# Kernel tuning notes

Hardware: AMD Instinct MI355X
Metric: run time of the kernel (lower is better)

## Reference

```python
import jax, jax.numpy as jnp
import numpy as np

B, Q, KV = 8, 16, 2048
NQ, NK, NV, H = 512, 512, 512, 512

def setup_inputs() -> dict:
    key = jax.random.key(0)
    k = jax.random.split(key, 7)
    s = 0.02
    return {
        "query": jax.random.normal(k[0], (B, Q, NQ), jnp.float32),
        "keys": jax.random.normal(k[1], (B, KV, NK), jnp.float32),
        "values": jax.random.normal(k[2], (B, KV, NV), jnp.float32),
        "W_weight": jax.random.normal(k[3], (H, NQ + NK), jnp.float32) * s,
        "W_bias": jax.random.normal(k[4], (H,), jnp.float32) * s,
        "v_weight": jax.random.normal(k[5], (1, H), jnp.float32) * s,
        "v_bias": jax.random.normal(k[6], (1,), jnp.float32) * s,
    }

def reference(query, keys, values, W_weight, W_bias, v_weight, v_bias):
    # Split W over the concat axis: cat([query, keys]) @ W^T == query@Wq^T + keys@Wk^T
    Wq = W_weight[:, :NQ]   # [H, Nq]
    Wk = W_weight[:, NQ:]   # [H, Nk]
    q_part = jnp.einsum('bqn,hn->bqh', query, Wq)   # [B,Q,H]
    k_part = jnp.einsum('bkn,hn->bkh', keys, Wk)    # [B,KV,H]
    # broadcast-add -> [B,KV,Q,H], tanh, project to scalar energy
    energy = jnp.tanh(k_part[:, :, None, :] + q_part[:, None, :, :] + W_bias)
    e = jnp.einsum('bkqh,h->bkq', energy, v_weight[0]) + v_bias[0]  # [B,KV,Q]
    scores = jax.nn.softmax(e, axis=1)              # softmax over KV
    # output = (values^T @ scores)^T -> [B,Q,Nv]
    output = jnp.einsum('bkn,bkq->bqn', values, scores)
    return output
```

## Files before the change

### kernel.cpp

```cpp
#include <hip/hip_runtime.h>
#include <cstddef>

using bf16x8  = __attribute__((ext_vector_type(8))) short;
using f32x4   = __attribute__((ext_vector_type(4))) float;
using ushort8 = __attribute__((ext_vector_type(8))) unsigned short;

#define GLL16(gp, lp) __builtin_amdgcn_global_load_lds( \
    (const __attribute__((address_space(1))) unsigned int*)(const void*)(gp), \
    (__attribute__((address_space(3))) unsigned int*)(void*)(lp), 16, 0, 0)

__device__ __forceinline__ float exp2_f(float x){ float r; asm("v_exp_f32 %0, %1" : "=v"(r) : "v"(x)); return r; }
__device__ __forceinline__ float rcp_f (float x){ float r; asm("v_rcp_f32 %0, %1" : "=v"(r) : "v"(x)); return r; }
__device__ __forceinline__ unsigned pk2(float lo, float hi){
  unsigned r; asm("v_cvt_pk_bf16_f32 %0, %1, %2" : "=v"(r) : "v"(lo), "v"(hi)); return r;
}
__device__ __forceinline__ unsigned short f2bf(float f){
  unsigned int u = __float_as_uint(f);
  u = u + 0x7FFFu + ((u >> 16) & 1u);
  return (unsigned short)(u >> 16);
}

#define KEYS_N   8388608
#define QG_BLOCKS 16
#define CONV_BLOCKS 4224
#define SCALE_2LOG2E 2.885390081777927f

#define OFF_KEYS_BF   0u
#define OFF_WK_BF     16777216u
#define OFF_EQB       17301504u
#define OFF_EPART     17563648u
#define OFF_SC        21757952u

__global__ __launch_bounds__(256) void k_convert(
    const float* __restrict__ keys, const float* __restrict__ W,
    const float* __restrict__ query,
    unsigned short* __restrict__ keys_bf, unsigned short* __restrict__ wk_bf,
    float* __restrict__ eqb)
{
  __shared__ short qg[128*32 + 32*32];
  if (blockIdx.x < QG_BLOCKS) {
    const int n0 = blockIdx.x * 32;
    const int tid = threadIdx.x;
    const int l = tid & 63, w = tid >> 6;
    short* A  = qg;
    short* Bs = qg + 4096;
    const int sub = tid >> 3;
    const int c4  = (tid & 7) * 4;
    const int wm = w & 1, wn = w >> 1;
    const int fr = l & 15, fg = l >> 4;

    f32x4 acc[4];
    #pragma unroll
    for (int i = 0; i < 4; ++i) acc[i] = (f32x4){0.f,0.f,0.f,0.f};

    float4 a4[4], b4, a4n[4], b4n;
    #pragma unroll
    for (int m = 0; m < 4; ++m)
      a4[m] = *(const float4*)(query + (size_t)(m * 32 + sub) * 512 + c4);
    b4 = *(const float4*)(W + (size_t)(n0 + sub) * 1024 + c4);

    for (int kt = 0; kt < 16; ++kt) {
      if (kt < 15) {
        const int k0 = (kt + 1) * 32;
        #pragma unroll
        for (int m = 0; m < 4; ++m)
          a4n[m] = *(const float4*)(query + (size_t)(m * 32 + sub) * 512 + k0 + c4);
        b4n = *(const float4*)(W + (size_t)(n0 + sub) * 1024 + k0 + c4);
      }
      __syncthreads();
      #pragma unroll
      for (int m = 0; m < 4; ++m) {
        const int row = m * 32 + sub;
        const int o = row * 32 + (((c4 >> 3) ^ ((row >> 1) & 3)) << 3) + (c4 & 7);
        *(uint2*)&A[o] = make_uint2(pk2(a4[m].x, a4[m].y), pk2(a4[m].z, a4[m].w));
      }
      {
        const int o = sub * 32 + (((c4 >> 3) ^ ((sub >> 1) & 3)) << 3) + (c4 & 7);
        *(uint2*)&Bs[o] = make_uint2(pk2(b4.x, b4.y), pk2(b4.z, b4.w));
      }
      __syncthreads();
      bf16x8 af[4], bfv;
      #pragma unroll
      for (int i = 0; i < 4; ++i) {
        const int ar = wm*64 + i*16 + fr;
        af[i] = *(const bf16x8*)&A[ar*32 + ((fg ^ ((ar>>1)&3)) << 3)];
      }
      const int br = wn*16 + fr;
      bfv = *(const bf16x8*)&Bs[br*32 + ((fg ^ ((br>>1)&3)) << 3)];
      #pragma unroll
      for (int i = 0; i < 4; ++i)
        acc[i] = __builtin_amdgcn_mfma_f32_16x16x32_bf16(af[i], bfv, acc[i], 0, 0, 0);
      if (kt < 15) {
        #pragma unroll
        for (int m = 0; m < 4; ++m) a4[m] = a4n[m];
        b4 = b4n;
      }
    }
    const int gh = n0 + wn*16 + fr;
    #pragma unroll
    for (int i = 0; i < 4; ++i)
      #pragma unroll
      for (int r = 0; r < 4; ++r) {
        const int gm = wm*64 + i*16 + fg*4 + r;
        eqb[gm * 512 + gh] = exp2_f(acc[i][r] * SCALE_2LOG2E);
      }
    return;
  }
  int idx = ((blockIdx.x - QG_BLOCKS) * 256 + threadIdx.x) * 8;
  const float* src;
  unsigned short* dst;
  if (idx < KEYS_N) { src = keys + idx; dst = keys_bf + idx; }
  else {
    int e = idx - KEYS_N;
    src = W + (size_t)(e >> 9) * 1024 + 512 + (e & 511);
    dst = wk_bf + e;
  }
  float4 a = *(const float4*)src;
  float4 b = *(const float4*)(src + 4);
  ushort8 o;
  o[0]=f2bf(a.x); o[1]=f2bf(a.y); o[2]=f2bf(a.z); o[3]=f2bf(a.w);
  o[4]=f2bf(b.x); o[5]=f2bf(b.y); o[6]=f2bf(b.z); o[7]=f2bf(b.w);
  *(ushort8*)dst = o;
}

struct FusedSM {
  union {
    struct { short A[2][8192]; short B[2][8192]; } g;
    float ekf[128 * 128];
  } u;
};

__global__ __launch_bounds__(256, 2) void k_fused(
    const unsigned short* __restrict__ keys_bf, const unsigned short* __restrict__ wk_bf,
    const float* __restrict__ w_bias, const float* __restrict__ eqb,
    const float* __restrict__ vw, float* __restrict__ e_part)
{
  __shared__ FusedSM sm;
  const int tid = threadIdx.x;
  const int l = tid & 63, w = tid >> 6;
  const int by = blockIdx.x;
  const int hc = blockIdx.y;
  const int h0 = hc * 128;
  const int b  = by >> 4;

  const unsigned short* Aptr = keys_bf + (size_t)by * 128 * 512;
  const unsigned short* Bptr = wk_bf + (size_t)h0 * 512;

  const int srow = w * 32 + (l >> 3);
  const int scol = ((l & 7) ^ (l >> 3)) * 8;
  const int wm = w >> 1, wn = w & 1;
  const int fr = l & 15, fg = l >> 4;
  const int axk = fr & 7;

  f32x4 acc[4][4];
  #pragma unroll
  for (int i = 0; i < 4; ++i)
    #pragma unroll
    for (int j = 0; j < 4; ++j) acc[i][j] = (f32x4){0.f,0.f,0.f,0.f};

  auto stage = [&](int buf, int kt) {
    const int k0 = kt * 64;
    #pragma unroll
    for (int r = 0; r < 4; ++r) {
      GLL16(Aptr + (srow + r * 8) * 512 + k0 + scol, &sm.u.g.A[buf][w * 2048 + r * 512]);
      GLL16(Bptr + (srow + r * 8) * 512 + k0 + scol, &sm.u.g.B[buf][w * 2048 + r * 512]);
    }
  };
  auto compute = [&](int buf) {
    #pragma unroll
    for (int ks = 0; ks < 2; ++ks) {
      bf16x8 af[4], bfv[4];
      #pragma unroll
      for (int i = 0; i < 4; ++i) {
        af[i]  = *(const bf16x8*)&sm.u.g.A[buf][(wm*64 + i*16 + fr) * 64 + ((ks*4 + fg) ^ axk) * 8];
        bfv[i] = *(const bf16x8*)&sm.u.g.B[buf][(wn*64 + i*16 + fr) * 64 + ((ks*4 + fg) ^ axk) * 8];
      }
      #pragma unroll
      for (int i = 0; i < 4; ++i)
        #pragma unroll
        for (int j = 0; j < 4; ++j)
          acc[i][j] = __builtin_amdgcn_mfma_f32_16x16x32_bf16(af[i], bfv[j], acc[i][j], 0, 0, 0);
    }
  };

  stage(0, 0);
  #pragma unroll 1
  for (int kt = 0; kt < 8; ++kt) {
    if (kt < 7) {
      stage((kt + 1) & 1, kt + 1);
      asm volatile("s_waitcnt vmcnt(8)" ::: "memory");
    } else {
      asm volatile("s_waitcnt vmcnt(0)" ::: "memory");
    }
    __builtin_amdgcn_sched_barrier(0);
    __builtin_amdgcn_s_barrier();
    __builtin_amdgcn_sched_barrier(0);
    compute(kt & 1);
    asm volatile("s_waitcnt lgkmcnt(0)" ::: "memory");
    __builtin_amdgcn_sched_barrier(0);
    __builtin_amdgcn_s_barrier();
    __builtin_amdgcn_sched_barrier(0);
  }

  #pragma unroll
  for (int j = 0; j < 4; ++j) {
    const int col = wn*64 + j*16 + fr;
    const float bias = w_bias[h0 + col];
    const int chunk = col >> 3, coff = col & 7;
    #pragma unroll
    for (int i = 0; i < 4; ++i)
      #pragma unroll
      for (int r = 0; r < 4; ++r) {
        const int row = wm*64 + i*16 + fg*4 + r;
        const int key = ((row & 3) << 2) | ((row >> 2) & 3);
        sm.u.ekf[row * 128 + ((chunk ^ key) << 3) + coff] =
            exp2_f((acc[i][j][r] + bias) * SCALE_2LOG2E);
      }
  }

  const int ql = l >> 2, g = l & 3;
  float eq[32], vv[32];
  #pragma unroll
  for (int s = 0; s < 4; ++s)
    #pragma unroll
    for (int hf = 0; hf < 2; ++hf) {
      const int c = h0 + s*32 + hf*16 + g*4;
      const float4 e4 = *(const float4*)(eqb + (size_t)(b * 16 + ql) * 512 + c);
      const float4 v4 = *(const float4*)(vw + c);
      const int o = s*8 + hf*4;
      eq[o+0]=e4.x; eq[o+1]=e4.y; eq[o+2]=e4.z; eq[o+3]=e4.w;
      vv[o+0]=-2.f*v4.x; vv[o+1]=-2.f*v4.y; vv[o+2]=-2.f*v4.z; vv[o+3]=-2.f*v4.w;
    }
  __syncthreads();

  #pragma unroll 2
  for (int kk = 0; kk < 16; ++kk) {
    const int k0 = w * 32 + kk, k1 = k0 + 16;
    const int key = ((kk & 3) << 2) | ((kk >> 2) & 3);
    float a0 = 0.f, a1 = 0.f;
    #pragma unroll
    for (int s = 0; s < 4; ++s)
      #pragma unroll
      for (int hf = 0; hf < 2; ++hf) {
        const int ck = (4*s + 2*hf + (g >> 1)) ^ key;
        const int off = (ck << 3) + (g & 1) * 4;
        const float4 E0 = *(const float4*)&sm.u.ekf[k0 * 128 + off];
        const float4 E1 = *(const float4*)&sm.u.ekf[k1 * 128 + off];
        const int o = s*8 + hf*4;
        a0 = fmaf(vv[o+0], rcp_f(fmaf(E0.x, eq[o+0], 1.f)), a0);
        a0 = fmaf(vv[o+1], rcp_f(fmaf(E0.y, eq[o+1], 1.f)), a0);
        a0 = fmaf(vv[o+2], rcp_f(fmaf(E0.z, eq[o+2], 1.f)), a0);
        a0 = fmaf(vv[o+3], rcp_f(fmaf(E0.w, eq[o+3], 1.f)), a0);
        a1 = fmaf(vv[o+0], rcp_f(fmaf(E1.x, eq[o+0], 1.f)), a1);
        a1 = fmaf(vv[o+1], rcp_f(fmaf(E1.y, eq[o+1], 1.f)), a1);
        a1 = fmaf(vv[o+2], rcp_f(fmaf(E1.z, eq[o+2], 1.f)), a1);
        a1 = fmaf(vv[o+3], rcp_f(fmaf(E1.w, eq[o+3], 1.f)), a1);
      }
    a0 += __shfl_xor(a0, 1, 64);
    a0 += __shfl_xor(a0, 2, 64);
    a1 += __shfl_xor(a1, 1, 64);
    a1 += __shfl_xor(a1, 2, 64);
    if (g == 0) {
      e_part[(size_t)hc * 262144 + ((size_t)(by * 128 + k0)) * 16 + ql] = a0;
      e_part[(size_t)hc * 262144 + ((size_t)(by * 128 + k1)) * 16 + ql] = a1;
    }
  }
}

__global__ __launch_bounds__(256) void k_softmax(
    const float* __restrict__ e_part, float* __restrict__ sc)
{
  const int b = blockIdx.x >> 4, q = blockIdx.x & 15;
  const int base = b * 32768 + q;
  const int tid = threadIdx.x;
  __shared__ float redm[4], reds[4];

  float vals[8];
  float mx = -1e30f;
  #pragma unroll
  for (int i = 0; i < 8; ++i) {
    const int x = base + (tid + i * 256) * 16;
    vals[i] = (e_part[x] + e_part[x + 262144]) + (e_part[x + 524288] + e_part[x + 786432]);
    mx = fmaxf(mx, vals[i]);
  }
  #pragma unroll
  for (int msk = 1; msk < 64; msk <<= 1) mx = fmaxf(mx, __shfl_xor(mx, msk, 64));
  if ((tid & 63) == 0) redm[tid >> 6] = mx;
  __syncthreads();
  mx = fmaxf(fmaxf(redm[0], redm[1]), fmaxf(redm[2], redm[3]));

  float ex[8], sum = 0.f;
  #pragma unroll
  for (int i = 0; i < 8; ++i) { ex[i] = __expf(vals[i] - mx); sum += ex[i]; }
  #pragma unroll
  for (int msk = 1; msk < 64; msk <<= 1) sum += __shfl_xor(sum, msk, 64);
  if ((tid & 63) == 0) reds[tid >> 6] = sum;
  __syncthreads();
  sum = reds[0] + reds[1] + reds[2] + reds[3];
  const float r = 1.f / sum;
  #pragma unroll
  for (int i = 0; i < 8; ++i) sc[base + (tid + i * 256) * 16] = ex[i] * r;
}

__global__ __launch_bounds__(512) void k_pv(
    const float* __restrict__ values, const float* __restrict__ sc,
    float* __restrict__ out)
{
  __shared__ float lds[128 * 20];
  const int tid = threadIdx.x;
  const int nc = blockIdx.x & 31, b = blockIdx.x >> 5;
  const int n = tid & 15, kg = tid >> 4;
  const int l = tid & 63, w = tid >> 6;
  const int n0 = nc * 16;

  float acc[16];
  #pragma unroll
  for (int q = 0; q < 16; ++q) acc[q] = 0.f;

  for (int kc = 0; kc < 16; ++kc) {
    __syncthreads();
    {
      const float* ssrc = sc + (size_t)(b * 2048 + kc * 128) * 16;
      const int row = tid >> 2, c4 = (tid & 3) * 4;
      *(float4*)&lds[row * 20 + c4] = *(const float4*)&ssrc[row * 16 + c4];
    }
    __syncthreads();
    const float* vb = values + ((size_t)(b * 2048 + kc * 128 + kg * 4)) * 512 + n0 + n;
    #pragma unroll
    for (int k2 = 0; k2 < 4; ++k2) {
      const float v = vb[(size_t)k2 * 512];
      const float* sr = &lds[(kg * 4 + k2) * 20];
      #pragma unroll
      for (int qq = 0; qq < 4; ++qq) {
        const float4 s4 = *(const float4*)&sr[qq * 4];
        acc[qq*4+0] = fmaf(v, s4.x, acc[qq*4+0]);
        acc[qq*4+1] = fmaf(v, s4.y, acc[qq*4+1]);
        acc[qq*4+2] = fmaf(v, s4.z, acc[qq*4+2]);
        acc[qq*4+3] = fmaf(v, s4.w, acc[qq*4+3]);
      }
    }
  }
  #pragma unroll
  for (int q = 0; q < 16; ++q) {
    acc[q] += __shfl_xor(acc[q], 16, 64);
    acc[q] += __shfl_xor(acc[q], 32, 64);
  }
  __syncthreads();
  if (l < 16) {
    #pragma unroll
    for (int q = 0; q < 16; ++q) lds[w * 256 + q * 16 + l] = acc[q];
  }
  __syncthreads();
  if (tid < 256) {
    const int q = tid >> 4, nn = tid & 15;
    float s = 0.f;
    #pragma unroll
    for (int w2 = 0; w2 < 8; ++w2) s += lds[w2 * 256 + q * 16 + nn];
    out[((size_t)(b * 16 + q)) * 512 + n0 + nn] = s;
  }
}

extern "C" void kernel_launch(void* const* d_in, const int* in_sizes, int n_in,
                              void* d_out, int out_size, void* d_ws, size_t ws_size,
                              hipStream_t stream)
{
  const float* query  = (const float*)d_in[0];
  const float* keys   = (const float*)d_in[1];
  const float* values = (const float*)d_in[2];
  const float* W      = (const float*)d_in[3];
  const float* w_bias = (const float*)d_in[4];
  const float* vw     = (const float*)d_in[5];

  char* ws = (char*)d_ws;
  unsigned short* keys_bf = (unsigned short*)(ws + OFF_KEYS_BF);
  unsigned short* wk_bf   = (unsigned short*)(ws + OFF_WK_BF);
  float* eqb    = (float*)(ws + OFF_EQB);
  float* e_part = (float*)(ws + OFF_EPART);
  float* sc     = (float*)(ws + OFF_SC);

  hipLaunchKernelGGL(k_convert, dim3(QG_BLOCKS + CONV_BLOCKS), dim3(256), 0, stream,
                     keys, W, query, keys_bf, wk_bf, eqb);
  hipLaunchKernelGGL(k_fused, dim3(128, 4), dim3(256), 0, stream,
                     keys_bf, wk_bf, w_bias, eqb, vw, e_part);
  hipLaunchKernelGGL(k_softmax, dim3(128), dim3(256), 0, stream, e_part, sc);
  hipLaunchKernelGGL(k_pv, dim3(256), dim3(512), 0, stream, values, sc, (float*)d_out);
}
```

Baseline: 87.33 us.

## Split fused GEMM+energy kernel into separate GEMM and energy kernels

```diff
diff --git a/kernel.cpp b/kernel.cpp
--- a/kernel.cpp
+++ b/kernel.cpp
@@ -28,8 +28,9 @@
 #define OFF_KEYS_BF   0u
 #define OFF_WK_BF     16777216u
 #define OFF_EQB       17301504u
-#define OFF_EPART     17563648u
-#define OFF_SC        21757952u
+#define OFF_EKB       17563648u
+#define OFF_EPART     51118080u
+#define OFF_SC        55312384u
 
 __global__ __launch_bounds__(256) void k_convert(
     const float* __restrict__ keys, const float* __restrict__ W,
@@ -123,25 +124,18 @@
   *(ushort8*)dst = o;
 }
 
-struct FusedSM {
-  union {
-    struct { short A[2][8192]; short B[2][8192]; } g;
-    float ekf[128 * 128];
-  } u;
-};
-
-__global__ __launch_bounds__(256, 2) void k_fused(
+struct GemmSM { short A[2][8192]; short B[2][8192]; };
+
+__global__ __launch_bounds__(256, 2) void k_gemm(
     const unsigned short* __restrict__ keys_bf, const unsigned short* __restrict__ wk_bf,
-    const float* __restrict__ w_bias, const float* __restrict__ eqb,
-    const float* __restrict__ vw, float* __restrict__ e_part)
-{
-  __shared__ FusedSM sm;
+    const float* __restrict__ w_bias, float* __restrict__ ekb)
+{
+  __shared__ GemmSM sm;
   const int tid = threadIdx.x;
   const int l = tid & 63, w = tid >> 6;
   const int by = blockIdx.x;
   const int hc = blockIdx.y;
   const int h0 = hc * 128;
-  const int b  = by >> 4;
 
   const unsigned short* Aptr = keys_bf + (size_t)by * 128 * 512;
   const unsigned short* Bptr = wk_bf + (size_t)h0 * 512;
@@ -162,8 +156,8 @@
     const int k0 = kt * 64;
     #pragma unroll
     for (int r = 0; r < 4; ++r) {
-      GLL16(Aptr + (srow + r * 8) * 512 + k0 + scol, &sm.u.g.A[buf][w * 2048 + r * 512]);
-      GLL16(Bptr + (srow + r * 8) * 512 + k0 + scol, &sm.u.g.B[buf][w * 2048 + r * 512]);
+      GLL16(Aptr + (srow + r * 8) * 512 + k0 + scol, &sm.A[buf][w * 2048 + r * 512]);
+      GLL16(Bptr + (srow + r * 8) * 512 + k0 + scol, &sm.B[buf][w * 2048 + r * 512]);
     }
   };
   auto compute = [&](int buf) {
@@ -172,8 +166,8 @@
       bf16x8 af[4], bfv[4];
       #pragma unroll
       for (int i = 0; i < 4; ++i) {
-        af[i]  = *(const bf16x8*)&sm.u.g.A[buf][(wm*64 + i*16 + fr) * 64 + ((ks*4 + fg) ^ axk) * 8];
-        bfv[i] = *(const bf16x8*)&sm.u.g.B[buf][(wn*64 + i*16 + fr) * 64 + ((ks*4 + fg) ^ axk) * 8];
+        af[i]  = *(const bf16x8*)&sm.A[buf][(wm*64 + i*16 + fr) * 64 + ((ks*4 + fg) ^ axk) * 8];
+        bfv[i] = *(const bf16x8*)&sm.B[buf][(wn*64 + i*16 + fr) * 64 + ((ks*4 + fg) ^ axk) * 8];
       }
       #pragma unroll
       for (int i = 0; i < 4; ++i)
@@ -206,64 +200,80 @@
   for (int j = 0; j < 4; ++j) {
     const int col = wn*64 + j*16 + fr;
     const float bias = w_bias[h0 + col];
-    const int chunk = col >> 3, coff = col & 7;
     #pragma unroll
     for (int i = 0; i < 4; ++i)
       #pragma unroll
       for (int r = 0; r < 4; ++r) {
         const int row = wm*64 + i*16 + fg*4 + r;
-        const int key = ((row & 3) << 2) | ((row >> 2) & 3);
-        sm.u.ekf[row * 128 + ((chunk ^ key) << 3) + coff] =
+        ekb[(size_t)(by * 128 + row) * 512 + h0 + col] =
             exp2_f((acc[i][j][r] + bias) * SCALE_2LOG2E);
       }
   }
+}
+
+__global__ __launch_bounds__(256, 6) void k_energy(
+    const float* __restrict__ ekb, const float* __restrict__ eqb,
+    const float* __restrict__ vw, float* __restrict__ e_part)
+{
+  __shared__ float ekt[32 * 128];
+  __shared__ float vvs[128];
+  const int tid = threadIdx.x;
+  const int l = tid & 63, w = tid >> 6;
+  const int by2 = blockIdx.x;
+  const int hc = blockIdx.y;
+  const int h0 = hc * 128;
+  const int b = by2 >> 6;
+
+  {
+    const float* src = ekb + (size_t)by2 * 32 * 512 + h0;
+    #pragma unroll
+    for (int m = 0; m < 4; ++m) {
+      const int e4b = m * 256 + w * 64;
+      const int e4 = e4b + l;
+      const int row = e4 >> 5, c4 = (e4 & 31) * 4;
+      GLL16(src + (size_t)row * 512 + c4, &ekt[e4b * 4]);
+    }
+  }
+  if (tid < 32) {
+    const float4 v4 = *(const float4*)(vw + h0 + tid * 4);
+    vvs[tid*4+0] = -2.f*v4.x; vvs[tid*4+1] = -2.f*v4.y;
+    vvs[tid*4+2] = -2.f*v4.z; vvs[tid*4+3] = -2.f*v4.w;
+  }
 
   const int ql = l >> 2, g = l & 3;
-  float eq[32], vv[32];
+  float eq[32];
   #pragma unroll
   for (int s = 0; s < 4; ++s)
     #pragma unroll
     for (int hf = 0; hf < 2; ++hf) {
-      const int c = h0 + s*32 + hf*16 + g*4;
-      const float4 e4 = *(const float4*)(eqb + (size_t)(b * 16 + ql) * 512 + c);
-      const float4 v4 = *(const float4*)(vw + c);
+      const float4 e4 = *(const float4*)(eqb + (size_t)(b * 16 + ql) * 512
+                                         + h0 + s*32 + hf*16 + g*4);
       const int o = s*8 + hf*4;
       eq[o+0]=e4.x; eq[o+1]=e4.y; eq[o+2]=e4.z; eq[o+3]=e4.w;
-      vv[o+0]=-2.f*v4.x; vv[o+1]=-2.f*v4.y; vv[o+2]=-2.f*v4.z; vv[o+3]=-2.f*v4.w;
     }
   __syncthreads();
 
   #pragma unroll 2
-  for (int kk = 0; kk < 16; ++kk) {
-    const int k0 = w * 32 + kk, k1 = k0 + 16;
-    const int key = ((kk & 3) << 2) | ((kk >> 2) & 3);
-    float a0 = 0.f, a1 = 0.f;
+  for (int rr = 0; rr < 8; ++rr) {
+    const int row = w * 8 + rr;
+    float a = 0.f;
     #pragma unroll
     for (int s = 0; s < 4; ++s)
       #pragma unroll
       for (int hf = 0; hf < 2; ++hf) {
-        const int ck = (4*s + 2*hf + (g >> 1)) ^ key;
-        const int off = (ck << 3) + (g & 1) * 4;
-        const float4 E0 = *(const float4*)&sm.u.ekf[k0 * 128 + off];
-        const float4 E1 = *(const float4*)&sm.u.ekf[k1 * 128 + off];
+        const int c = s*32 + hf*16 + g*4;
+        const float4 E = *(const float4*)&ekt[row * 128 + c];
+        const float4 V = *(const float4*)&vvs[c];
         const int o = s*8 + hf*4;
-        a0 = fmaf(vv[o+0], rcp_f(fmaf(E0.x, eq[o+0], 1.f)), a0);
-        a0 = fmaf(vv[o+1], rcp_f(fmaf(E0.y, eq[o+1], 1.f)), a0);
-        a0 = fmaf(vv[o+2], rcp_f(fmaf(E0.z, eq[o+2], 1.f)), a0);
-        a0 = fmaf(vv[o+3], rcp_f(fmaf(E0.w, eq[o+3], 1.f)), a0);
-        a1 = fmaf(vv[o+0], rcp_f(fmaf(E1.x, eq[o+0], 1.f)), a1);
-        a1 = fmaf(vv[o+1], rcp_f(fmaf(E1.y, eq[o+1], 1.f)), a1);
-        a1 = fmaf(vv[o+2], rcp_f(fmaf(E1.z, eq[o+2], 1.f)), a1);
-        a1 = fmaf(vv[o+3], rcp_f(fmaf(E1.w, eq[o+3], 1.f)), a1);
-      }
-    a0 += __shfl_xor(a0, 1, 64);
-    a0 += __shfl_xor(a0, 2, 64);
-    a1 += __shfl_xor(a1, 1, 64);
-    a1 += __shfl_xor(a1, 2, 64);
-    if (g == 0) {
-      e_part[(size_t)hc * 262144 + ((size_t)(by * 128 + k0)) * 16 + ql] = a0;
-      e_part[(size_t)hc * 262144 + ((size_t)(by * 128 + k1)) * 16 + ql] = a1;
-    }
+        a = fmaf(V.x, rcp_f(fmaf(E.x, eq[o+0], 1.f)), a);
+        a = fmaf(V.y, rcp_f(fmaf(E.y, eq[o+1], 1.f)), a);
+        a = fmaf(V.z, rcp_f(fmaf(E.z, eq[o+2], 1.f)), a);
+        a = fmaf(V.w, rcp_f(fmaf(E.w, eq[o+3], 1.f)), a);
+      }
+    a += __shfl_xor(a, 1, 64);
+    a += __shfl_xor(a, 2, 64);
+    if (g == 0)
+      e_part[(size_t)hc * 262144 + ((size_t)(by2 * 32 + row)) * 16 + ql] = a;
   }
 }
 
@@ -375,13 +385,16 @@
   unsigned short* keys_bf = (unsigned short*)(ws + OFF_KEYS_BF);
   unsigned short* wk_bf   = (unsigned short*)(ws + OFF_WK_BF);
   float* eqb    = (float*)(ws + OFF_EQB);
+  float* ekb    = (float*)(ws + OFF_EKB);
   float* e_part = (float*)(ws + OFF_EPART);
   float* sc     = (float*)(ws + OFF_SC);
 
   hipLaunchKernelGGL(k_convert, dim3(QG_BLOCKS + CONV_BLOCKS), dim3(256), 0, stream,
                      keys, W, query, keys_bf, wk_bf, eqb);
-  hipLaunchKernelGGL(k_fused, dim3(128, 4), dim3(256), 0, stream,
-                     keys_bf, wk_bf, w_bias, eqb, vw, e_part);
+  hipLaunchKernelGGL(k_gemm, dim3(128, 4), dim3(256), 0, stream,
+                     keys_bf, wk_bf, w_bias, ekb);
+  hipLaunchKernelGGL(k_energy, dim3(512, 4), dim3(256), 0, stream,
+                     ekb, eqb, vw, e_part);
   hipLaunchKernelGGL(k_softmax, dim3(128), dim3(256), 0, stream, e_part, sc);
   hipLaunchKernelGGL(k_pv, dim3(256), dim3(512), 0, stream, values, sc, (float*)d_out);
 }
```

Result: slower. 89.62 us (+2.6%).
